# Performance work log

Hardware: AMD Instinct MI355X
Metric: run time of the kernel (lower is better)

Reference implementation:

```python
import jax, jax.numpy as jnp
import numpy as np

B, C, H, W = 8, 768, 32, 32
NH = 12
HD = C // NH
HID = 4 * C
EPS = 1e-5


def _layer_norm(x, g, b):
    mu = jnp.mean(x, axis=-1, keepdims=True)
    var = jnp.mean(jnp.square(x - mu), axis=-1, keepdims=True)
    return (x - mu) * jax.lax.rsqrt(var + EPS) * g + b


def setup_inputs() -> dict:
    key = jax.random.key(0)
    ks = jax.random.split(key, 12)
    s = 0.02
    return {
        "x": jax.random.normal(ks[0], (B, C, H, W), jnp.float32),
        "conv_w": jax.random.normal(ks[1], (C, 1, 3, 3), jnp.float32) * s,  # depthwise OIHW
        "conv_b": jnp.zeros((C,), jnp.float32),
        "ln1_g": jnp.ones((C,), jnp.float32),
        "ln1_b": jnp.zeros((C,), jnp.float32),
        "qkv_w": jax.random.normal(ks[2], (3 * C, C), jnp.float32) * s,  # no bias (qkv_bias=False)
        "proj_w": jax.random.normal(ks[3], (C, C), jnp.float32) * s,
        "proj_b": jnp.zeros((C,), jnp.float32),
        "ln2_g": jnp.ones((C,), jnp.float32),
        "ln2_b": jnp.zeros((C,), jnp.float32),
        "fc1_w": jax.random.normal(ks[4], (HID, C), jnp.float32) * s,
        "fc1_b": jnp.zeros((HID,), jnp.float32),
        "fc2_w": jax.random.normal(ks[5], (C, HID), jnp.float32) * s,
        "fc2_b": jnp.zeros((C,), jnp.float32),
    }


def reference(x, conv_w, conv_b, ln1_g, ln1_b, qkv_w, proj_w, proj_b,
              ln2_g, ln2_b, fc1_w, fc1_b, fc2_w, fc2_b):
    # depthwise 3x3 conv positional embedding, residual
    pe = jax.lax.conv_general_dilated(
        x, conv_w, window_strides=(1, 1), padding=((1, 1), (1, 1)),
        dimension_numbers=("NCHW", "OIHW", "NCHW"), feature_group_count=C)
    x = x + pe + conv_b[None, :, None, None]

    b, c, h, w = x.shape
    t = x.reshape(b, c, h * w).transpose(0, 2, 1)  # [B, N, C]

    # attention
    hn = _layer_norm(t, ln1_g, ln1_b)
    qkv = hn @ qkv_w.T  # [B, N, 3C]
    qkv = qkv.reshape(b, h * w, 3, NH, HD).transpose(2, 0, 3, 1, 4)  # [3, B, nh, N, hd]
    q, k, v = qkv[0], qkv[1], qkv[2]
    scale = HD ** -0.5
    attn = jax.nn.softmax(jnp.einsum("bhnd,bhmd->bhnm", q, k) * scale, axis=-1)
    o = jnp.einsum("bhnm,bhmd->bhnd", attn, v).transpose(0, 2, 1, 3).reshape(b, h * w, c)
    t = t + (o @ proj_w.T + proj_b)

    # MLP
    hn = _layer_norm(t, ln2_g, ln2_b)
    hid = jax.nn.gelu(hn @ fc1_w.T + fc1_b, approximate=False)
    t = t + (hid @ fc2_w.T + fc2_b)

    return t.transpose(0, 2, 1).reshape(b, c, h, w)
```

## Files before the change

kernel.cpp:

```cpp
#include <hip/hip_runtime.h>
#include <math.h>


typedef __bf16 bf16;
typedef __attribute__((ext_vector_type(8))) __bf16 bf16x8;
typedef __attribute__((ext_vector_type(4))) __bf16 bf16x4;
typedef __attribute__((ext_vector_type(4))) float f32x4;

#define B_   8
#define C_   768
#define N_   1024
#define NH_  12
#define HD_  64
#define HID_ 3072
#define NTOK   (B_ * N_)
#define NHEADS (B_ * NH_)
#define FA_C   0.1803368801111601f

__device__ __forceinline__ void gload_lds16(const void* g, void* l) {
  __builtin_amdgcn_global_load_lds(
      (__attribute__((address_space(1))) void*)(void*)g,
      (__attribute__((address_space(3))) void*)l, 16, 0, 0);
}

__device__ __forceinline__ float gelu1(float x) {
  float u = 0.7978845608028654f * x * (1.0f + 0.044715f * x * x);
  float e = __builtin_amdgcn_exp2f(u * 2.885390081777927f);
  float th = 1.0f - 2.0f * __builtin_amdgcn_rcpf(e + 1.0f);
  return 0.5f * x * (1.0f + th);
}

#define PIPE_SYNC(N)                                              \
  do {                                                            \
    asm volatile("s_waitcnt vmcnt(" #N ") lgkmcnt(0)" ::: "memory"); \
    __builtin_amdgcn_sched_barrier(0);                            \
    __builtin_amdgcn_s_barrier();                                 \
    __builtin_amdgcn_sched_barrier(0);                            \
    asm volatile("" ::: "memory");                                \
  } while (0)

#define BAR_FENCED()                                              \
  do {                                                            \
    __builtin_amdgcn_sched_barrier(0);                            \
    __builtin_amdgcn_s_barrier();                                 \
    __builtin_amdgcn_sched_barrier(0);                            \
  } while (0)
#define LGKM0()                                                   \
  do {                                                            \
    asm volatile("s_waitcnt lgkmcnt(0)" ::: "memory");            \
    __builtin_amdgcn_sched_barrier(0);                            \
  } while (0)

__global__ __launch_bounds__(512) void gemm_fc2(
    const bf16* __restrict__ A, const bf16* __restrict__ Bw,
    const float* __restrict__ bias, const float* __restrict__ resid,
    float* __restrict__ outp, int K, int lda, int ldb) {
  __shared__ __align__(16) char smem[122880];
  const int tid = threadIdx.x;
  const int wave = tid >> 6, lane = tid & 63;
  const int wr = wave & 1, wc = wave >> 1;
  const int lr = lane & 15, kq = lane >> 4;

  const int bid = blockIdx.x;
  const int g = bid & 7, s = bid >> 3;
  const int ms = s >> 2;
  const int m0 = (g * 8 + ms) * 128;
  const int n0 = (s & 3) * 192;

  f32x4 acc[4][3];
#pragma unroll
  for (int i = 0; i < 4; ++i)
#pragma unroll
    for (int j = 0; j < 3; ++j) acc[i][j] = (f32x4){0.f, 0.f, 0.f, 0.f};

  const bf16* pa[2];
  const bf16* pb[3];
  int da[2], db[3];
#pragma unroll
  for (int c = 0; c < 2; ++c) {
    const int sidx = c * 512 + tid;
    const int r = sidx >> 3, seg = (sidx & 7) ^ (r & 7);
    pa[c] = A + (size_t)(m0 + r) * lda + seg * 8;
    da[c] = sidx * 16;
  }
#pragma unroll
  for (int c = 0; c < 3; ++c) {
    const int sidx = c * 512 + tid;
    const int r = sidx >> 3, seg = (sidx & 7) ^ (r & 7);
    pb[c] = Bw + (size_t)(n0 + r) * ldb + seg * 8;
    db[c] = 16384 + sidx * 16;
  }

  const int NT = K >> 6;

#pragma unroll
  for (int tt = 0; tt < 2; ++tt) {
    char* wb = smem + tt * 40960;
    gload_lds16(pb[0], wb + db[0]);
    gload_lds16(pb[1], wb + db[1]);
    gload_lds16(pb[2], wb + db[2]);
    gload_lds16(pa[0], wb + da[0]);
    gload_lds16(pa[1], wb + da[1]);
    pb[0] += 64; pb[1] += 64; pb[2] += 64; pa[0] += 64; pa[1] += 64;
  }

  int cur = 0;
  for (int t = 0; t < NT - 1; ++t) {
    const char* rb = smem + cur * 40960;
    int wi = cur + 2; if (wi >= 3) wi -= 3;
    char* wb = smem + wi * 40960;
    const bool dostage = (t < NT - 2);

    asm volatile("s_waitcnt vmcnt(5) lgkmcnt(0)" ::: "memory");
    BAR_FENCED();

    bf16x8 af[4], bf[3];
#pragma unroll
    for (int i = 0; i < 4; ++i) {
      const int r = wr * 64 + i * 16 + lr;
      af[i] = *(const bf16x8*)(rb + (r * 8 + (kq ^ (r & 7))) * 16);
    }
#pragma unroll
    for (int j = 0; j < 3; ++j) {
      const int r = wc * 48 + j * 16 + lr;
      bf[j] = *(const bf16x8*)(rb + 16384 + (r * 8 + (kq ^ (r & 7))) * 16);
    }
    if (dostage) {
      gload_lds16(pb[0], wb + db[0]); pb[0] += 64;
      gload_lds16(pb[1], wb + db[1]); pb[1] += 64;
      gload_lds16(pb[2], wb + db[2]); pb[2] += 64;
    }
    BAR_FENCED();
    LGKM0();
    __builtin_amdgcn_s_setprio(1);
#pragma unroll
    for (int i = 0; i < 4; ++i)
#pragma unroll
      for (int j = 0; j < 3; ++j)
        acc[i][j] = __builtin_amdgcn_mfma_f32_16x16x32_bf16(bf[j], af[i],
                                                            acc[i][j], 0, 0, 0);
    __builtin_amdgcn_s_setprio(0);
    BAR_FENCED();

#pragma unroll
    for (int i = 0; i < 4; ++i) {
      const int r = wr * 64 + i * 16 + lr;
      af[i] = *(const bf16x8*)(rb + (r * 8 + ((4 + kq) ^ (r & 7))) * 16);
    }
#pragma unroll
    for (int j = 0; j < 3; ++j) {
      const int r = wc * 48 + j * 16 + lr;
      bf[j] = *(const bf16x8*)(rb + 16384 + (r * 8 + ((4 + kq) ^ (r & 7))) * 16);
    }
    if (dostage) {
      gload_lds16(pa[0], wb + da[0]); pa[0] += 64;
      gload_lds16(pa[1], wb + da[1]); pa[1] += 64;
    }
    BAR_FENCED();
    LGKM0();
    __builtin_amdgcn_s_setprio(1);
#pragma unroll
    for (int i = 0; i < 4; ++i)
#pragma unroll
      for (int j = 0; j < 3; ++j)
        acc[i][j] = __builtin_amdgcn_mfma_f32_16x16x32_bf16(bf[j], af[i],
                                                            acc[i][j], 0, 0, 0);
    __builtin_amdgcn_s_setprio(0);
    BAR_FENCED();

    if (++cur == 3) cur = 0;
  }

  {
    const char* rb = smem + cur * 40960;
    bf16x8 af[4], bf[3];
    asm volatile("s_waitcnt vmcnt(0) lgkmcnt(0)" ::: "memory");
    BAR_FENCED();
#pragma unroll
    for (int kh = 0; kh < 2; ++kh) {
      const int c0 = kh * 4 + kq;
#pragma unroll
      for (int i = 0; i < 4; ++i) {
        const int r = wr * 64 + i * 16 + lr;
        af[i] = *(const bf16x8*)(rb + (r * 8 + (c0 ^ (r & 7))) * 16);
      }
#pragma unroll
      for (int j = 0; j < 3; ++j) {
        const int r = wc * 48 + j * 16 + lr;
        bf[j] = *(const bf16x8*)(rb + 16384 + (r * 8 + (c0 ^ (r & 7))) * 16);
      }
      __builtin_amdgcn_s_setprio(1);
#pragma unroll
      for (int i = 0; i < 4; ++i)
#pragma unroll
        for (int j = 0; j < 3; ++j)
          acc[i][j] = __builtin_amdgcn_mfma_f32_16x16x32_bf16(bf[j], af[i],
                                                              acc[i][j], 0, 0, 0);
      __builtin_amdgcn_s_setprio(0);
    }
  }

  {
    float* tile = (float*)smem;
    const int b = m0 >> 10, tok0 = m0 & (N_ - 1);
#pragma unroll
    for (int sl = 0; sl < 3; ++sl) {
      __syncthreads();
#pragma unroll
      for (int j = 0; j < 3; ++j) {
        const int nl0 = wc * 48 + j * 16 + kq * 4;
        if (((wc * 48 + j * 16) >> 6) == sl) {
          const int n = n0 + nl0;
          const f32x4 bv = *(const f32x4*)(bias + n);
#pragma unroll
          for (int i = 0; i < 4; ++i) {
            const int ml = wr * 64 + i * 16 + lr;
            const float* rp = resid + (size_t)(m0 + ml) * C_ + n;
            f32x4 old = *(const f32x4*)rp;
            const f32x4 v = acc[i][j];
#pragma unroll
            for (int r = 0; r < 4; ++r)
              tile[(nl0 - sl * 64 + r) * 132 + ml] = old[r] + v[r] + bv[r];
          }
        }
      }
      __syncthreads();
      const int nl = tid & 63, mc = tid >> 6;
      float* dst = outp + ((size_t)(b * C_ + n0 + sl * 64 + nl)) * N_ +
                   tok0 + mc * 16;
      const float* src = tile + nl * 132 + mc * 16;
#pragma unroll
      for (int q = 0; q < 4; ++q)
        *(f32x4*)(dst + q * 4) = *(const f32x4*)(src + q * 4);
    }
  }
}

__global__ __launch_bounds__(512) void gemm_fc1(
    const bf16* __restrict__ A, const bf16* __restrict__ Bw,
    const float* __restrict__ bias, bf16* __restrict__ outp,
    int K, int lda, int ldb, int ntiles, int mtpx, int ldo) {
  __shared__ __align__(16) char smem[114688];
  const int tid = threadIdx.x;
  const int wave = tid >> 6, lane = tid & 63;
  const int wr = wave & 1, wc = wave >> 1;
  const int lr = lane & 15, kq = lane >> 4;

  const int bid = blockIdx.x;
  const int g = bid & 7, s = bid >> 3;
  const int ms = s / ntiles;
  const int m0 = (g * mtpx + ms) * 256;
  const int n0 = (s - ms * ntiles) * 192;

  f32x4 acc[8][3];
#pragma unroll
  for (int i = 0; i < 8; ++i)
#pragma unroll
    for (int j = 0; j < 3; ++j) acc[i][j] = (f32x4){0.f, 0.f, 0.f, 0.f};

  const bf16* pa[4];
  const bf16* pb[3];
  int da[4], db[3];
#pragma unroll
  for (int c = 0; c < 4; ++c) {
    const int sidx = c * 512 + tid;
    const int r = sidx >> 3, seg = (sidx & 7) ^ (r & 7);
    pa[c] = A + (size_t)(m0 + r) * lda + seg * 8;
    da[c] = sidx * 16;
  }
#pragma unroll
  for (int c = 0; c < 3; ++c) {
    const int sidx = c * 512 + tid;
    const int r = sidx >> 3, seg = (sidx & 7) ^ (r & 7);
    pb[c] = Bw + (size_t)(n0 + r) * ldb + seg * 8;
    db[c] = 32768 + sidx * 16;
  }

  const int NT = K >> 6;

  gload_lds16(pb[0], smem + db[0]);
  gload_lds16(pb[1], smem + db[1]);
  gload_lds16(pb[2], smem + db[2]);
  gload_lds16(pa[0], smem + da[0]);
  gload_lds16(pa[1], smem + da[1]);
  gload_lds16(pa[2], smem + da[2]);
  gload_lds16(pa[3], smem + da[3]);
#pragma unroll
  for (int c = 0; c < 4; ++c) pa[c] += 64;
#pragma unroll
  for (int c = 0; c < 3; ++c) pb[c] += 64;

  for (int t = 0; t < NT - 1; ++t) {
    const char* rb = smem + (t & 1) * 57344;
    char* wb = smem + ((t & 1) ^ 1) * 57344;
    bf16x8 af[4], bf0[3], bf1[3];

    PIPE_SYNC(1);
#pragma unroll
    for (int i = 0; i < 4; ++i) {
      const int r = wr * 128 + i * 16 + lr;
      af[i] = *(const bf16x8*)(rb + (r * 8 + (kq ^ (r & 7))) * 16);
    }
#pragma unroll
    for (int j = 0; j < 3; ++j) {
      const int r = wc * 48 + j * 16 + lr;
      bf0[j] = *(const bf16x8*)(rb + 32768 + (r * 8 + (kq ^ (r & 7))) * 16);
    }
    gload_lds16(pb[0], wb + db[0]); pb[0] += 64;
    gload_lds16(pb[1], wb + db[1]); pb[1] += 64;
    __builtin_amdgcn_s_setprio(1);
#pragma unroll
    for (int i = 0; i < 4; ++i)
#pragma unroll
      for (int j = 0; j < 3; ++j)
        acc[i][j] = __builtin_amdgcn_mfma_f32_16x16x32_bf16(bf0[j], af[i],
                                                            acc[i][j], 0, 0, 0);
    __builtin_amdgcn_s_setprio(0);

    PIPE_SYNC(2);
#pragma unroll
    for (int i = 0; i < 4; ++i) {
      const int r = wr * 128 + 64 + i * 16 + lr;
      af[i] = *(const bf16x8*)(rb + (r * 8 + (kq ^ (r & 7))) * 16);
    }
    gload_lds16(pb[2], wb + db[2]); pb[2] += 64;
    gload_lds16(pa[0], wb + da[0]); pa[0] += 64;
    __builtin_amdgcn_s_setprio(1);
#pragma unroll
    for (int i = 0; i < 4; ++i)
#pragma unroll
      for (int j = 0; j < 3; ++j)
        acc[4 + i][j] = __builtin_amdgcn_mfma_f32_16x16x32_bf16(
            bf0[j], af[i], acc[4 + i][j], 0, 0, 0);
    __builtin_amdgcn_s_setprio(0);

    PIPE_SYNC(4);
#pragma unroll
    for (int i = 0; i < 4; ++i) {
      const int r = wr * 128 + i * 16 + lr;
      af[i] = *(const bf16x8*)(rb + (r * 8 + ((4 + kq) ^ (r & 7))) * 16);
    }
#pragma unroll
    for (int j = 0; j < 3; ++j) {
      const int r = wc * 48 + j * 16 + lr;
      bf1[j] = *(const bf16x8*)(rb + 32768 + (r * 8 + ((4 + kq) ^ (r & 7))) * 16);
    }
    gload_lds16(pa[1], wb + da[1]); pa[1] += 64;
    gload_lds16(pa[2], wb + da[2]); pa[2] += 64;
    __builtin_amdgcn_s_setprio(1);
#pragma unroll
    for (int i = 0; i < 4; ++i)
#pragma unroll
      for (int j = 0; j < 3; ++j)
        acc[i][j] = __builtin_amdgcn_mfma_f32_16x16x32_bf16(bf1[j], af[i],
                                                            acc[i][j], 0, 0, 0);
    __builtin_amdgcn_s_setprio(0);

    PIPE_SYNC(6);
#pragma unroll
    for (int i = 0; i < 4; ++i) {
      const int r = wr * 128 + 64 + i * 16 + lr;
      af[i] = *(const bf16x8*)(rb + (r * 8 + ((4 + kq) ^ (r & 7))) * 16);
    }
    gload_lds16(pa[3], wb + da[3]); pa[3] += 64;
    __builtin_amdgcn_s_setprio(1);
#pragma unroll
    for (int i = 0; i < 4; ++i)
#pragma unroll
      for (int j = 0; j < 3; ++j)
        acc[4 + i][j] = __builtin_amdgcn_mfma_f32_16x16x32_bf16(
            bf1[j], af[i], acc[4 + i][j], 0, 0, 0);
    __builtin_amdgcn_s_setprio(0);
  }

  {
    const char* rb = smem + ((NT - 1) & 1) * 57344;
    bf16x8 af[4], bf0[3], bf1[3];
    PIPE_SYNC(0);
#pragma unroll
    for (int j = 0; j < 3; ++j) {
      const int r = wc * 48 + j * 16 + lr;
      bf0[j] = *(const bf16x8*)(rb + 32768 + (r * 8 + (kq ^ (r & 7))) * 16);
      bf1[j] = *(const bf16x8*)(rb + 32768 + (r * 8 + ((4 + kq) ^ (r & 7))) * 16);
    }
    __builtin_amdgcn_s_setprio(1);
#pragma unroll
    for (int half = 0; half < 2; ++half) {
#pragma unroll
      for (int i = 0; i < 4; ++i) {
        const int r = wr * 128 + half * 64 + i * 16 + lr;
        af[i] = *(const bf16x8*)(rb + (r * 8 + (kq ^ (r & 7))) * 16);
      }
#pragma unroll
      for (int i = 0; i < 4; ++i)
#pragma unroll
        for (int j = 0; j < 3; ++j)
          acc[half * 4 + i][j] = __builtin_amdgcn_mfma_f32_16x16x32_bf16(
              bf0[j], af[i], acc[half * 4 + i][j], 0, 0, 0);
#pragma unroll
      for (int i = 0; i < 4; ++i) {
        const int r = wr * 128 + half * 64 + i * 16 + lr;
        af[i] = *(const bf16x8*)(rb + (r * 8 + ((4 + kq) ^ (r & 7))) * 16);
      }
#pragma unroll
      for (int i = 0; i < 4; ++i)
#pragma unroll
        for (int j = 0; j < 3; ++j)
          acc[half * 4 + i][j] = __builtin_amdgcn_mfma_f32_16x16x32_bf16(
              bf1[j], af[i], acc[half * 4 + i][j], 0, 0, 0);
    }
    __builtin_amdgcn_s_setprio(0);
  }

#pragma unroll
  for (int j = 0; j < 3; ++j) {
    const int n = n0 + wc * 48 + j * 16 + kq * 4;
    const f32x4 bv = *(const f32x4*)(bias + n);
#pragma unroll
    for (int i = 0; i < 8; ++i) {
      const int m = m0 + wr * 128 + i * 16 + lr;
      const f32x4 v = acc[i][j];
      bf16x4 pk = {(bf16)gelu1(v[0] + bv[0]), (bf16)gelu1(v[1] + bv[1]),
                   (bf16)gelu1(v[2] + bv[2]), (bf16)gelu1(v[3] + bv[3])};
      *(bf16x4*)(outp + (size_t)m * ldo + n) = pk;
    }
  }
}

template <int BN, int EPI, bool REMAP>
__global__ __launch_bounds__(256) void gemm_bt(
    const bf16* __restrict__ A, const bf16* __restrict__ B, int K, int lda,
    int ldb, int ntiles, bf16* __restrict__ o0, bf16* __restrict__ o1,
    bf16* __restrict__ o2, float* __restrict__ resid,
    const float* __restrict__ bias, float* __restrict__ outp) {
  constexpr int JJ = BN / 32;
  constexpr int BCH = BN / 32;
  constexpr int STAGE_B = (128 + BN) * 64 * 2;
  constexpr int EXTRA_B = (EPI == 0 ? 128 * 256 : 0);
  constexpr int SMEM_B = STAGE_B > EXTRA_B ? STAGE_B : EXTRA_B;
  __shared__ __align__(16) char smemraw[SMEM_B];
  bf16* As = (bf16*)smemraw;
  bf16* Bs = As + 128 * 64;

  const int tid = threadIdx.x;
  const int wave = tid >> 6, lane = tid & 63;
  const int wm = wave & 1, wn = wave >> 1;
  const int lr = lane & 15, kq = lane >> 4;
  const int sw = lr & 7;

  int m0, n0;
  if constexpr (REMAP) {
    const int bid = blockIdx.x;
    const int g = bid & 7, s = bid >> 3;
    const int ms = s / ntiles;
    m0 = (g * 8 + ms) * 128;
    n0 = (s - ms * ntiles) * BN;
  } else {
    m0 = blockIdx.y * 128;
    n0 = blockIdx.x * BN;
  }

  f32x4 acc[4][JJ];
#pragma unroll
  for (int i = 0; i < 4; i++)
#pragma unroll
    for (int j = 0; j < JJ; j++) acc[i][j] = (f32x4){0.f, 0.f, 0.f, 0.f};

  const bf16* ap[4];
  const bf16* bp[BCH];
  {
    const bf16* Arow = A + (size_t)m0 * lda;
    const bf16* Brow = B + (size_t)n0 * ldb;
#pragma unroll
    for (int it = 0; it < 4; ++it) {
      int s = it * 256 + tid;
      int r = s >> 3, seg = (s & 7) ^ (r & 7);
      ap[it] = Arow + (size_t)r * lda + seg * 8;
    }
#pragma unroll
    for (int it = 0; it < BCH; ++it) {
      int s = it * 256 + tid;
      int r = s >> 3, seg = (s & 7) ^ (r & 7);
      bp[it] = Brow + (size_t)r * ldb + seg * 8;
    }
  }

  for (int k0 = 0; k0 < K; k0 += 64) {
#pragma unroll
    for (int it = 0; it < 4; ++it) {
      gload_lds16(ap[it], (char*)As + (it * 256 + tid) * 16);
      ap[it] += 64;
    }
#pragma unroll
    for (int it = 0; it < BCH; ++it) {
      gload_lds16(bp[it], (char*)Bs + (it * 256 + tid) * 16);
      bp[it] += 64;
    }
    __syncthreads();

#pragma unroll
    for (int h = 0; h < 2; ++h) {
      bf16x8 af[4], bfr[JJ];
      const int c = h * 4 + kq;
#pragma unroll
      for (int i = 0; i < 4; i++) {
        int row = wm * 64 + i * 16 + lr;
        af[i] = *(const bf16x8*)((char*)As + (row * 8 + (c ^ sw)) * 16);
      }
#pragma unroll
      for (int j = 0; j < JJ; j++) {
        int row = wn * (BN / 2) + j * 16 + lr;
        bfr[j] = *(const bf16x8*)((char*)Bs + (row * 8 + (c ^ sw)) * 16);
      }
#pragma unroll
      for (int i = 0; i < 4; i++)
#pragma unroll
        for (int j = 0; j < JJ; j++)
          acc[i][j] = __builtin_amdgcn_mfma_f32_16x16x32_bf16(bfr[j], af[i],
                                                              acc[i][j], 0, 0, 0);
    }
    __syncthreads();
  }

  if constexpr (EPI == 0) {
    const int b = m0 >> 10, tok0 = m0 & (N_ - 1);
    if (n0 < 2 * C_) {
      const int s = n0 >= C_ ? 1 : 0;
      bf16* dst = s ? o1 : o0;
#pragma unroll
      for (int i = 0; i < 4; i++) {
        const int m = m0 + wm * 64 + i * 16 + lr;
#pragma unroll
        for (int j = 0; j < JJ; j++) {
          const int rem = n0 - s * C_ + wn * (BN / 2) + j * 16 + kq * 4;
          const int h = rem >> 6, d = rem & 63;
          const f32x4 v = acc[i][j];
          bf16x4 pk = {(bf16)v[0], (bf16)v[1], (bf16)v[2], (bf16)v[3]};
          size_t head = (size_t)b * NH_ + h;
          *(bf16x4*)(dst + (head * N_ + (m & (N_ - 1))) * HD_ + d) = pk;
        }
      }
    } else {
      bf16* tile = (bf16*)smemraw;
#pragma unroll
      for (int i = 0; i < 4; i++) {
        const int ml = wm * 64 + i * 16 + lr;
        const int mc = ml >> 3, mo = ml & 7;
#pragma unroll
        for (int j = 0; j < JJ; j++) {
          const f32x4 v = acc[i][j];
#pragma unroll
          for (int r = 0; r < 4; r++) {
            const int nl = wn * (BN / 2) + j * 16 + kq * 4 + r;
            *(bf16*)((char*)tile + nl * 256 + ((mc ^ (nl & 15)) * 16) + mo * 2) =
                (bf16)v[r];
          }
        }
      }
      __syncthreads();
      const int nl = tid >> 1, mh = (tid & 1) * 64;
      const int vb = n0 - 2 * C_ + nl;
      const size_t head = (size_t)b * NH_ + (vb >> 6);
      bf16* dst = o2 + (head * HD_ + (vb & 63)) * N_ + tok0 + mh;
#pragma unroll
      for (int c8 = 0; c8 < 8; ++c8) {
        const int c = (mh >> 3) + c8;
        bf16x8 val = *(const bf16x8*)((char*)tile + nl * 256 +
                                      ((c ^ (nl & 15)) * 16));
        *(bf16x8*)(dst + c8 * 8) = val;
      }
    }
  } else if constexpr (EPI == 3) {
#pragma unroll
    for (int j = 0; j < JJ; j++) {
      const int n = n0 + wn * (BN / 2) + j * 16 + kq * 4;
      const f32x4 bv = *(const f32x4*)(bias + n);
#pragma unroll
      for (int i = 0; i < 4; i++) {
        const int m = m0 + wm * 64 + i * 16 + lr;
        float* rp = resid + (size_t)m * C_ + n;
        f32x4 old = *(const f32x4*)rp;
        const f32x4 v = acc[i][j];
        f32x4 nw = {old[0] + v[0] + bv[0], old[1] + v[1] + bv[1],
                    old[2] + v[2] + bv[2], old[3] + v[3] + bv[3]};
        *(f32x4*)rp = nw;
      }
    }
  }
}

__global__ __launch_bounds__(256, 3) void flash_attn(
    const bf16* __restrict__ Qb, const bf16* __restrict__ Kb,
    const bf16* __restrict__ Vt, bf16* __restrict__ attn) {
  __shared__ __align__(16) bf16 ksm[2][64 * 64];
  __shared__ __align__(16) bf16 vsm[2][64 * 64];
  __shared__ __align__(16) bf16 psm[4][32 * 64];

  const int tid = threadIdx.x, wave = tid >> 6, lane = tid & 63;
  const int lr = lane & 15, kq = lane >> 4;
  const int head = blockIdx.y;
  const int b = head / NH_, hh = head - b * NH_;
  const int q0 = blockIdx.x * 128;
  const bf16* Qh = Qb + (size_t)head * (N_ * HD_);
  const bf16* Kh = Kb + (size_t)head * (N_ * HD_);
  const bf16* Vh = Vt + (size_t)head * (HD_ * N_);
  char* pw = (char*)&psm[wave][0];

  bf16x8 qf[2][2];
#pragma unroll
  for (int j = 0; j < 2; ++j)
#pragma unroll
    for (int kh = 0; kh < 2; ++kh)
      qf[j][kh] = *(const bf16x8*)(Qh +
                                   (size_t)(q0 + wave * 32 + j * 16 + lr) * HD_ +
                                   kh * 32 + kq * 8);

  f32x4 o[4][2];
#pragma unroll
  for (int i = 0; i < 4; i++)
#pragma unroll
    for (int j = 0; j < 2; j++) o[i][j] = (f32x4){0.f, 0.f, 0.f, 0.f};
  float mprev[2] = {-1e30f, -1e30f}, lacc[2] = {0.f, 0.f};

  auto stage = [&](int t, int bi) {
#pragma unroll
    for (int it = 0; it < 2; ++it) {
      int s = it * 256 + tid;
      int r = s >> 3, seg = (s & 7) ^ (r & 7);
      gload_lds16(Kh + (size_t)(t * 64 + r) * HD_ + seg * 8,
                  (char*)ksm[bi] + (it * 256 + wave * 64) * 16);
    }
#pragma unroll
    for (int it = 0; it < 2; ++it) {
      int s = it * 256 + tid;
      int r = s >> 3, seg = (s & 7) ^ (r & 7);
      gload_lds16(Vh + (size_t)r * N_ + t * 64 + seg * 8,
                  (char*)vsm[bi] + (it * 256 + wave * 64) * 16);
    }
  };

  stage(0, 0);

  for (int t = 0; t < 16; ++t) {
    const int bi = t & 1;
    __syncthreads();
    if (t < 15) stage(t + 1, bi ^ 1);

    f32x4 sacc[4][2];
#pragma unroll
    for (int i = 0; i < 4; ++i) {
#pragma unroll
      for (int j = 0; j < 2; ++j) sacc[i][j] = (f32x4){0.f, 0.f, 0.f, 0.f};
      int row = i * 16 + lr;
      bf16x8 kf0 = *(const bf16x8*)((char*)ksm[bi] + row * 128 +
                                    ((kq ^ (row & 7)) * 16));
      bf16x8 kf1 = *(const bf16x8*)((char*)ksm[bi] + row * 128 +
                                    (((4 + kq) ^ (row & 7)) * 16));
#pragma unroll
      for (int j = 0; j < 2; ++j) {
        sacc[i][j] = __builtin_amdgcn_mfma_f32_16x16x32_bf16(kf0, qf[j][0],
                                                             sacc[i][j], 0, 0, 0);
        sacc[i][j] = __builtin_amdgcn_mfma_f32_16x16x32_bf16(kf1, qf[j][1],
                                                             sacc[i][j], 0, 0, 0);
      }
    }

#pragma unroll
    for (int j = 0; j < 2; ++j) {
      float mx = -1e30f;
#pragma unroll
      for (int i = 0; i < 4; ++i)
#pragma unroll
        for (int r = 0; r < 4; ++r) mx = fmaxf(mx, sacc[i][j][r]);
      mx = fmaxf(mx, __shfl_xor(mx, 16));
      mx = fmaxf(mx, __shfl_xor(mx, 32));
      float mnew = fmaxf(mprev[j], mx);
      float alpha = __builtin_amdgcn_exp2f((mprev[j] - mnew) * FA_C);
      mprev[j] = mnew;
      float rs = 0.f;
      const int prow = j * 16 + lr;
#pragma unroll
      for (int i = 0; i < 4; ++i) {
        float p0 = __builtin_amdgcn_exp2f((sacc[i][j][0] - mnew) * FA_C);
        float p1 = __builtin_amdgcn_exp2f((sacc[i][j][1] - mnew) * FA_C);
        float p2 = __builtin_amdgcn_exp2f((sacc[i][j][2] - mnew) * FA_C);
        float p3 = __builtin_amdgcn_exp2f((sacc[i][j][3] - mnew) * FA_C);
        rs += (p0 + p1) + (p2 + p3);
        bf16x4 pk = {(bf16)p0, (bf16)p1, (bf16)p2, (bf16)p3};
        int c = i * 2 + (kq >> 1);
        *(bf16x4*)(pw + prow * 128 + ((c ^ (prow & 7)) * 16) + (kq & 1) * 8) = pk;
      }
      rs += __shfl_xor(rs, 16);
      rs += __shfl_xor(rs, 32);
      lacc[j] = lacc[j] * alpha + rs;
#pragma unroll
      for (int i = 0; i < 4; ++i) {
        o[i][j][0] *= alpha; o[i][j][1] *= alpha;
        o[i][j][2] *= alpha; o[i][j][3] *= alpha;
      }
    }

#pragma unroll
    for (int k0c = 0; k0c < 2; ++k0c) {
      bf16x8 pf[2];
#pragma unroll
      for (int j = 0; j < 2; ++j) {
        int prow = j * 16 + lr, c = k0c * 4 + kq;
        pf[j] = *(const bf16x8*)(pw + prow * 128 + ((c ^ (prow & 7)) * 16));
      }
#pragma unroll
      for (int i = 0; i < 4; ++i) {
        int d = i * 16 + lr, c = k0c * 4 + kq;
        bf16x8 vf = *(const bf16x8*)((char*)vsm[bi] + d * 128 +
                                     ((c ^ (d & 7)) * 16));
#pragma unroll
        for (int j = 0; j < 2; ++j)
          o[i][j] = __builtin_amdgcn_mfma_f32_16x16x32_bf16(vf, pf[j], o[i][j],
                                                            0, 0, 0);
      }
    }
  }

#pragma unroll
  for (int j = 0; j < 2; ++j) {
    float inv = 1.0f / lacc[j];
    int tok = q0 + wave * 32 + j * 16 + lr;
    bf16* op = attn + ((size_t)(b * N_ + tok)) * C_ + hh * HD_;
#pragma unroll
    for (int i = 0; i < 4; ++i) {
      bf16x4 pk = {(bf16)(o[i][j][0] * inv), (bf16)(o[i][j][1] * inv),
                   (bf16)(o[i][j][2] * inv), (bf16)(o[i][j][3] * inv)};
      *(bf16x4*)(op + i * 16 + kq * 4) = pk;
    }
  }
}

__global__ __launch_bounds__(256) void cast_all(
    const float* __restrict__ a, int na, const float* __restrict__ b, int nb,
    const float* __restrict__ c, int nc, const float* __restrict__ d,
    bf16* __restrict__ dst) {
  int i = (blockIdx.x * 256 + threadIdx.x) * 4;
  const float* src;
  int off;
  if (i < na) { src = a; off = i; }
  else if (i < na + nb) { src = b; off = i - na; }
  else if (i < na + nb + nc) { src = c; off = i - na - nb; }
  else { src = d; off = i - na - nb - nc; }
  float4 v = *(const float4*)(src + off);
  bf16x4 o = {(bf16)v.x, (bf16)v.y, (bf16)v.z, (bf16)v.w};
  *(bf16x4*)(dst + i) = o;
}

__global__ __launch_bounds__(256) void conv_pe_t(const float* __restrict__ x,
                                                 const float* __restrict__ cw,
                                                 const float* __restrict__ cb,
                                                 float* __restrict__ t0) {
  __shared__ float tile[32][33];
  const int h = blockIdx.x, ct = blockIdx.y, b = blockIdx.z;
  const int tid = threadIdx.x;
  const int w = tid & 31, cs = tid >> 5;
#pragma unroll
  for (int cc = cs; cc < 32; cc += 8) {
    int c = ct * 32 + cc;
    const float* xp = x + ((size_t)(b * C_ + c)) * 1024;
    const float* wp = cw + c * 9;
    float s = cb[c] + xp[h * 32 + w];
#pragma unroll
    for (int ky = 0; ky < 3; ++ky) {
      int hy = h + ky - 1;
      if ((unsigned)hy < 32u) {
#pragma unroll
        for (int kx = 0; kx < 3; ++kx) {
          int wx = w + kx - 1;
          if ((unsigned)wx < 32u) s += xp[hy * 32 + wx] * wp[ky * 3 + kx];
        }
      }
    }
    tile[cc][w] = s;
  }
  __syncthreads();
  const int cc = tid & 31;
#pragma unroll
  for (int wc = tid >> 5; wc < 32; wc += 8)
    t0[((size_t)(b * N_) + h * 32 + wc) * C_ + ct * 32 + cc] = tile[cc][wc];
}

__global__ __launch_bounds__(256) void ln_bf16(const float* __restrict__ t,
                                               const float* __restrict__ g,
                                               const float* __restrict__ be,
                                               bf16* __restrict__ out) {
  int row = blockIdx.x, tid = threadIdx.x;
  const float* p = t + (size_t)row * C_;
  float v0 = p[tid], v1 = p[tid + 256], v2 = p[tid + 512];
  __shared__ float rs[256], rq[256];
  rs[tid] = v0 + v1 + v2;
  rq[tid] = v0 * v0 + v1 * v1 + v2 * v2;
  __syncthreads();
  for (int off = 128; off; off >>= 1) {
    if (tid < off) {
      rs[tid] += rs[tid + off];
      rq[tid] += rq[tid + off];
    }
    __syncthreads();
  }
  float mu = rs[0] * (1.f / C_);
  float var = rq[0] * (1.f / C_) - mu * mu;
  float rstd = rsqrtf(var + 1e-5f);
  bf16* q = out + (size_t)row * C_;
  q[tid] = (bf16)((v0 - mu) * rstd * g[tid] + be[tid]);
  q[tid + 256] = (bf16)((v1 - mu) * rstd * g[tid + 256] + be[tid + 256]);
  q[tid + 512] = (bf16)((v2 - mu) * rstd * g[tid + 512] + be[tid + 512]);
}

extern "C" void kernel_launch(void* const* d_in, const int* in_sizes, int n_in,
                              void* d_out, int out_size, void* d_ws,
                              size_t ws_size, hipStream_t stream) {
  (void)in_sizes; (void)n_in; (void)out_size; (void)ws_size;
  const float* x      = (const float*)d_in[0];
  const float* conv_w = (const float*)d_in[1];
  const float* conv_b = (const float*)d_in[2];
  const float* ln1_g  = (const float*)d_in[3];
  const float* ln1_b  = (const float*)d_in[4];
  const float* qkv_w  = (const float*)d_in[5];
  const float* proj_w = (const float*)d_in[6];
  const float* proj_b = (const float*)d_in[7];
  const float* ln2_g  = (const float*)d_in[8];
  const float* ln2_b  = (const float*)d_in[9];
  const float* fc1_w  = (const float*)d_in[10];
  const float* fc1_b  = (const float*)d_in[11];
  const float* fc2_w  = (const float*)d_in[12];
  const float* fc2_b  = (const float*)d_in[13];
  float* out = (float*)d_out;

  char* w = (char*)d_ws;
  auto carve = [&](size_t bytes) {
    char* p = w;
    w += (bytes + 255) & ~(size_t)255;
    return p;
  };
  bf16* hid   = (bf16*)carve((size_t)NTOK * HID_ * 2);
  float* t0   = (float*)carve((size_t)NTOK * C_ * 4);
  bf16* lnout = (bf16*)carve((size_t)NTOK * C_ * 2);
  bf16* wq    = (bf16*)carve((size_t)3 * C_ * C_ * 2);
  bf16* wp    = (bf16*)carve((size_t)C_ * C_ * 2);
  bf16* w1    = (bf16*)carve((size_t)HID_ * C_ * 2);
  bf16* w2    = (bf16*)carve((size_t)C_ * HID_ * 2);
  bf16* Qb    = (bf16*)carve((size_t)NHEADS * N_ * HD_ * 2);
  bf16* Kb    = (bf16*)carve((size_t)NHEADS * N_ * HD_ * 2);
  bf16* Vt    = (bf16*)carve((size_t)NHEADS * HD_ * N_ * 2);
  bf16* attn  = (bf16*)carve((size_t)NTOK * C_ * 2);

  const int na = 3 * C_ * C_, nb = C_ * C_, nc = HID_ * C_, nd = C_ * HID_;
  cast_all<<<(na + nb + nc + nd) / 1024, 256, 0, stream>>>(
      qkv_w, na, proj_w, nb, fc1_w, nc, fc2_w, wq);

  conv_pe_t<<<dim3(32, C_ / 32, B_), 256, 0, stream>>>(x, conv_w, conv_b, t0);

  ln_bf16<<<NTOK, 256, 0, stream>>>(t0, ln1_g, ln1_b, lnout);
  gemm_bt<128, 0, true><<<1152, 256, 0, stream>>>(
      lnout, wq, 768, 768, 768, 18, Qb, Kb, Vt, nullptr, nullptr, nullptr);

  flash_attn<<<dim3(N_ / 128, NHEADS), 256, 0, stream>>>(Qb, Kb, Vt, attn);

  gemm_bt<64, 3, true><<<768, 256, 0, stream>>>(
      attn, wp, 768, 768, 768, 12, nullptr, nullptr, nullptr, t0, proj_b,
      nullptr);
  ln_bf16<<<NTOK, 256, 0, stream>>>(t0, ln2_g, ln2_b, lnout);
  gemm_fc1<<<512, 512, 0, stream>>>(lnout, w1, fc1_b, hid, 768, 768, 768,
                                    16, 4, HID_);
  gemm_fc2<<<256, 512, 0, stream>>>(hid, w2, fc2_b, t0, out, 3072, 3072, 3072);
}
```

Measured before the change: 386.2 us.

## Replace fc1 GEMM with 256x256-tile 8-phase pipelined kernel and simplify fc2 sync

The fc1 GEMM moves from 256x192 tiles to 256x256 tiles (384 blocks instead of 512). It uses a new four-quadrant schedule where each K step splits into phases that interleave partial LDS reads, global-to-LDS staging and MFMA blocks, with reuse of A/B fragments across quadrants. The aim is a higher MFMA-to-load ratio and better overlap of memory traffic with compute. fc2's main loop is also simplified: one PIPE_SYNC per K step, all staging issued up front, and the mid-iteration barriers removed. This cuts barrier overhead but depends on the triple-buffer distance for correctness, and the fc1 change raises register and LDS pressure.

```diff
diff --git a/kernel.cpp b/kernel.cpp
--- a/kernel.cpp
+++ b/kernel.cpp
@@ -50,6 +50,240 @@
     asm volatile("s_waitcnt lgkmcnt(0)" ::: "memory");            \
     __builtin_amdgcn_sched_barrier(0);                            \
   } while (0)
+#define WAITV4()                                                  \
+  do {                                                            \
+    asm volatile("s_waitcnt vmcnt(4)" ::: "memory");              \
+    __builtin_amdgcn_sched_barrier(0);                            \
+  } while (0)
+
+__global__ __launch_bounds__(512) void gemm_fc1_8ph(
+    const bf16* __restrict__ A, const bf16* __restrict__ Bw,
+    const float* __restrict__ bias, bf16* __restrict__ outp,
+    int K, int lda, int ldb, int ntiles, int mtpx, int ldo) {
+  __shared__ __align__(16) char smem[131072];
+  const int tid = threadIdx.x;
+  const int wave = tid >> 6, lane = tid & 63;
+  const int wr = wave & 1, wc = wave >> 1;
+  const int lr = lane & 15, kq = lane >> 4;
+
+  const int bid = blockIdx.x;
+  const int g = bid & 7, s = bid >> 3;
+  const int ms = s / ntiles;
+  const int m0 = (g * mtpx + ms) * 256;
+  const int n0 = (s - ms * ntiles) * 256;
+
+  f32x4 acc[8][4];
+#pragma unroll
+  for (int i = 0; i < 8; ++i)
+#pragma unroll
+    for (int j = 0; j < 4; ++j) acc[i][j] = (f32x4){0.f, 0.f, 0.f, 0.f};
+
+  const bf16* pa[2][2];
+  const bf16* pb[2][2];
+  int dof[2];
+#pragma unroll
+  for (int ld = 0; ld < 2; ++ld) {
+    const int sidx = ld * 512 + tid;
+    const int r = sidx >> 3, seg = (sidx & 7) ^ (r & 7);
+    pa[0][ld] = A + (size_t)(m0 + r) * lda + seg * 8;
+    pa[1][ld] = A + (size_t)(m0 + 128 + r) * lda + seg * 8;
+    pb[0][ld] = Bw + (size_t)(n0 + r) * ldb + seg * 8;
+    pb[1][ld] = Bw + (size_t)(n0 + 128 + r) * ldb + seg * 8;
+    dof[ld] = sidx * 16;
+  }
+
+  const int NT = K >> 6;
+
+  auto aread = [&](const char* base, int qm, int i, int k) -> bf16x8 {
+    const int ra = qm * 64 + i * 16 + lr;
+    const int c = k * 4 + kq;
+    return *(const bf16x8*)(base + wr * 16384 +
+                            (ra * 8 + (c ^ (ra & 7))) * 16);
+  };
+  auto bread = [&](const char* base, int qn, int j, int k) -> bf16x8 {
+    const int cb = wc * 64 + qn * 32 + j * 16;
+    const int hb = cb >> 7;
+    const int rl = (cb & 127) + lr;
+    const int c = k * 4 + kq;
+    return *(const bf16x8*)(base + 32768 + hb * 16384 +
+                            (rl * 8 + (c ^ (rl & 7))) * 16);
+  };
+
+  gload_lds16(pa[0][0], smem + dof[0]);
+  gload_lds16(pa[0][1], smem + dof[1]);
+  gload_lds16(pb[0][0], smem + 32768 + dof[0]);
+  gload_lds16(pb[0][1], smem + 32768 + dof[1]);
+  gload_lds16(pa[1][0], smem + 16384 + dof[0]);
+  gload_lds16(pa[1][1], smem + 16384 + dof[1]);
+  gload_lds16(pb[1][0], smem + 49152 + dof[0]);
+  gload_lds16(pb[1][1], smem + 49152 + dof[1]);
+#pragma unroll
+  for (int ld = 0; ld < 2; ++ld) {
+    pa[0][ld] += 64; pa[1][ld] += 64; pb[0][ld] += 64; pb[1][ld] += 64;
+  }
+  PIPE_SYNC(4);
+
+  for (int t = 0; t < NT - 1; ++t) {
+    const char* rb = smem + (t & 1) * 65536;
+    char* wb = smem + ((t & 1) ^ 1) * 65536;
+    bf16x8 af0[4][2], af1[4][2], bf0[2][2], bf1[2][2];
+
+#pragma unroll
+    for (int i = 0; i < 4; ++i)
+#pragma unroll
+      for (int k = 0; k < 2; ++k) af0[i][k] = aread(rb, 0, i, k);
+#pragma unroll
+    for (int j = 0; j < 2; ++j)
+#pragma unroll
+      for (int k = 0; k < 2; ++k) bf0[j][k] = bread(rb, 0, j, k);
+    gload_lds16(pa[0][0], wb + dof[0]); pa[0][0] += 64;
+    gload_lds16(pa[0][1], wb + dof[1]); pa[0][1] += 64;
+    WAITV4();
+    BAR_FENCED();
+    LGKM0();
+    __builtin_amdgcn_s_setprio(1);
+#pragma unroll
+    for (int k = 0; k < 2; ++k)
+#pragma unroll
+      for (int i = 0; i < 4; ++i)
+#pragma unroll
+        for (int j = 0; j < 2; ++j)
+          acc[i][j] = __builtin_amdgcn_mfma_f32_16x16x32_bf16(
+              bf0[j][k], af0[i][k], acc[i][j], 0, 0, 0);
+    __builtin_amdgcn_s_setprio(0);
+    BAR_FENCED();
+
+#pragma unroll
+    for (int i = 0; i < 4; ++i)
+#pragma unroll
+      for (int k = 0; k < 2; ++k) af1[i][k] = aread(rb, 1, i, k);
+    gload_lds16(pb[0][0], wb + 32768 + dof[0]); pb[0][0] += 64;
+    gload_lds16(pb[0][1], wb + 32768 + dof[1]); pb[0][1] += 64;
+    WAITV4();
+    BAR_FENCED();
+    LGKM0();
+    __builtin_amdgcn_s_setprio(1);
+#pragma unroll
+    for (int k = 0; k < 2; ++k)
+#pragma unroll
+      for (int i = 0; i < 4; ++i)
+#pragma unroll
+        for (int j = 0; j < 2; ++j)
+          acc[4 + i][j] = __builtin_amdgcn_mfma_f32_16x16x32_bf16(
+              bf0[j][k], af1[i][k], acc[4 + i][j], 0, 0, 0);
+    __builtin_amdgcn_s_setprio(0);
+    BAR_FENCED();
+
+#pragma unroll
+    for (int j = 0; j < 2; ++j)
+#pragma unroll
+      for (int k = 0; k < 2; ++k) bf1[j][k] = bread(rb, 1, j, k);
+    gload_lds16(pa[1][0], wb + 16384 + dof[0]); pa[1][0] += 64;
+    gload_lds16(pa[1][1], wb + 16384 + dof[1]); pa[1][1] += 64;
+    BAR_FENCED();
+    LGKM0();
+    __builtin_amdgcn_s_setprio(1);
+#pragma unroll
+    for (int k = 0; k < 2; ++k)
+#pragma unroll
+      for (int i = 0; i < 4; ++i)
+#pragma unroll
+        for (int j = 0; j < 2; ++j)
+          acc[i][2 + j] = __builtin_amdgcn_mfma_f32_16x16x32_bf16(
+              bf1[j][k], af0[i][k], acc[i][2 + j], 0, 0, 0);
+    __builtin_amdgcn_s_setprio(0);
+    BAR_FENCED();
+
+    gload_lds16(pb[1][0], wb + 49152 + dof[0]); pb[1][0] += 64;
+    gload_lds16(pb[1][1], wb + 49152 + dof[1]); pb[1][1] += 64;
+    WAITV4();
+    BAR_FENCED();
+    LGKM0();
+    __builtin_amdgcn_s_setprio(1);
+#pragma unroll
+    for (int k = 0; k < 2; ++k)
+#pragma unroll
+      for (int i = 0; i < 4; ++i)
+#pragma unroll
+        for (int j = 0; j < 2; ++j)
+          acc[4 + i][2 + j] = __builtin_amdgcn_mfma_f32_16x16x32_bf16(
+              bf1[j][k], af1[i][k], acc[4 + i][2 + j], 0, 0, 0);
+    __builtin_amdgcn_s_setprio(0);
+    BAR_FENCED();
+  }
+
+  {
+    const char* rb = smem + ((NT - 1) & 1) * 65536;
+    bf16x8 af0[4][2], af1[4][2], bf0[2][2], bf1[2][2];
+    PIPE_SYNC(0);
+#pragma unroll
+    for (int i = 0; i < 4; ++i)
+#pragma unroll
+      for (int k = 0; k < 2; ++k) af0[i][k] = aread(rb, 0, i, k);
+#pragma unroll
+    for (int j = 0; j < 2; ++j)
+#pragma unroll
+      for (int k = 0; k < 2; ++k) bf0[j][k] = bread(rb, 0, j, k);
+    LGKM0();
+    __builtin_amdgcn_s_setprio(1);
+#pragma unroll
+    for (int k = 0; k < 2; ++k)
+#pragma unroll
+      for (int i = 0; i < 4; ++i)
+#pragma unroll
+        for (int j = 0; j < 2; ++j)
+          acc[i][j] = __builtin_amdgcn_mfma_f32_16x16x32_bf16(
+              bf0[j][k], af0[i][k], acc[i][j], 0, 0, 0);
+    __builtin_amdgcn_s_setprio(0);
+#pragma unroll
+    for (int i = 0; i < 4; ++i)
+#pragma unroll
+      for (int k = 0; k < 2; ++k) af1[i][k] = aread(rb, 1, i, k);
+    LGKM0();
+    __builtin_amdgcn_s_setprio(1);
+#pragma unroll
+    for (int k = 0; k < 2; ++k)
+#pragma unroll
+      for (int i = 0; i < 4; ++i)
+#pragma unroll
+        for (int j = 0; j < 2; ++j)
+          acc[4 + i][j] = __builtin_amdgcn_mfma_f32_16x16x32_bf16(
+              bf0[j][k], af1[i][k], acc[4 + i][j], 0, 0, 0);
+    __builtin_amdgcn_s_setprio(0);
+#pragma unroll
+    for (int j = 0; j < 2; ++j)
+#pragma unroll
+      for (int k = 0; k < 2; ++k) bf1[j][k] = bread(rb, 1, j, k);
+    LGKM0();
+    __builtin_amdgcn_s_setprio(1);
+#pragma unroll
+    for (int k = 0; k < 2; ++k)
+#pragma unroll
+      for (int i = 0; i < 4; ++i)
+#pragma unroll
+        for (int j = 0; j < 2; ++j) {
+          acc[i][2 + j] = __builtin_amdgcn_mfma_f32_16x16x32_bf16(
+              bf1[j][k], af0[i][k], acc[i][2 + j], 0, 0, 0);
+          acc[4 + i][2 + j] = __builtin_amdgcn_mfma_f32_16x16x32_bf16(
+              bf1[j][k], af1[i][k], acc[4 + i][2 + j], 0, 0, 0);
+        }
+    __builtin_amdgcn_s_setprio(0);
+  }
+
+#pragma unroll
+  for (int j = 0; j < 4; ++j) {
+    const int n = n0 + wc * 64 + j * 16 + kq * 4;
+    const f32x4 bv = *(const f32x4*)(bias + n);
+#pragma unroll
+    for (int i = 0; i < 8; ++i) {
+      const int m = m0 + wr * 128 + i * 16 + lr;
+      const f32x4 v = acc[i][j];
+      bf16x4 pk = {(bf16)gelu1(v[0] + bv[0]), (bf16)gelu1(v[1] + bv[1]),
+                   (bf16)gelu1(v[2] + bv[2]), (bf16)gelu1(v[3] + bv[3])};
+      *(bf16x4*)(outp + (size_t)m * ldo + n) = pk;
+    }
+  }
+}
 
 __global__ __launch_bounds__(512) void gemm_fc2(
     const bf16* __restrict__ A, const bf16* __restrict__ Bw,
@@ -107,13 +341,16 @@
   int cur = 0;
   for (int t = 0; t < NT - 1; ++t) {
     const char* rb = smem + cur * 40960;
-    int wi = cur + 2; if (wi >= 3) wi -= 3;
-    char* wb = smem + wi * 40960;
-    const bool dostage = (t < NT - 2);
-
-    asm volatile("s_waitcnt vmcnt(5) lgkmcnt(0)" ::: "memory");
-    BAR_FENCED();
-
+    PIPE_SYNC(5);
+    if (t < NT - 2) {
+      int wi = cur + 2; if (wi >= 3) wi -= 3;
+      char* wb = smem + wi * 40960;
+      gload_lds16(pb[0], wb + db[0]); pb[0] += 64;
+      gload_lds16(pb[1], wb + db[1]); pb[1] += 64;
+      gload_lds16(pb[2], wb + db[2]); pb[2] += 64;
+      gload_lds16(pa[0], wb + da[0]); pa[0] += 64;
+      gload_lds16(pa[1], wb + da[1]); pa[1] += 64;
+    }
     bf16x8 af[4], bf[3];
 #pragma unroll
     for (int i = 0; i < 4; ++i) {
@@ -125,13 +362,6 @@
       const int r = wc * 48 + j * 16 + lr;
       bf[j] = *(const bf16x8*)(rb + 16384 + (r * 8 + (kq ^ (r & 7))) * 16);
     }
-    if (dostage) {
-      gload_lds16(pb[0], wb + db[0]); pb[0] += 64;
-      gload_lds16(pb[1], wb + db[1]); pb[1] += 64;
-      gload_lds16(pb[2], wb + db[2]); pb[2] += 64;
-    }
-    BAR_FENCED();
-    LGKM0();
     __builtin_amdgcn_s_setprio(1);
 #pragma unroll
     for (int i = 0; i < 4; ++i)
@@ -140,8 +370,6 @@
         acc[i][j] = __builtin_amdgcn_mfma_f32_16x16x32_bf16(bf[j], af[i],
                                                             acc[i][j], 0, 0, 0);
     __builtin_amdgcn_s_setprio(0);
-    BAR_FENCED();
-
 #pragma unroll
     for (int i = 0; i < 4; ++i) {
       const int r = wr * 64 + i * 16 + lr;
@@ -152,12 +380,6 @@
       const int r = wc * 48 + j * 16 + lr;
       bf[j] = *(const bf16x8*)(rb + 16384 + (r * 8 + ((4 + kq) ^ (r & 7))) * 16);
     }
-    if (dostage) {
-      gload_lds16(pa[0], wb + da[0]); pa[0] += 64;
-      gload_lds16(pa[1], wb + da[1]); pa[1] += 64;
-    }
-    BAR_FENCED();
-    LGKM0();
     __builtin_amdgcn_s_setprio(1);
 #pragma unroll
     for (int i = 0; i < 4; ++i)
@@ -166,16 +388,13 @@
         acc[i][j] = __builtin_amdgcn_mfma_f32_16x16x32_bf16(bf[j], af[i],
                                                             acc[i][j], 0, 0, 0);
     __builtin_amdgcn_s_setprio(0);
-    BAR_FENCED();
-
     if (++cur == 3) cur = 0;
   }
 
   {
     const char* rb = smem + cur * 40960;
     bf16x8 af[4], bf[3];
-    asm volatile("s_waitcnt vmcnt(0) lgkmcnt(0)" ::: "memory");
-    BAR_FENCED();
+    PIPE_SYNC(0);
 #pragma unroll
     for (int kh = 0; kh < 2; ++kh) {
       const int c0 = kh * 4 + kq;
@@ -232,197 +451,6 @@
 #pragma unroll
       for (int q = 0; q < 4; ++q)
         *(f32x4*)(dst + q * 4) = *(const f32x4*)(src + q * 4);
-    }
-  }
-}
-
-__global__ __launch_bounds__(512) void gemm_fc1(
-    const bf16* __restrict__ A, const bf16* __restrict__ Bw,
-    const float* __restrict__ bias, bf16* __restrict__ outp,
-    int K, int lda, int ldb, int ntiles, int mtpx, int ldo) {
-  __shared__ __align__(16) char smem[114688];
-  const int tid = threadIdx.x;
-  const int wave = tid >> 6, lane = tid & 63;
-  const int wr = wave & 1, wc = wave >> 1;
-  const int lr = lane & 15, kq = lane >> 4;
-
-  const int bid = blockIdx.x;
-  const int g = bid & 7, s = bid >> 3;
-  const int ms = s / ntiles;
-  const int m0 = (g * mtpx + ms) * 256;
-  const int n0 = (s - ms * ntiles) * 192;
-
-  f32x4 acc[8][3];
-#pragma unroll
-  for (int i = 0; i < 8; ++i)
-#pragma unroll
-    for (int j = 0; j < 3; ++j) acc[i][j] = (f32x4){0.f, 0.f, 0.f, 0.f};
-
-  const bf16* pa[4];
-  const bf16* pb[3];
-  int da[4], db[3];
-#pragma unroll
-  for (int c = 0; c < 4; ++c) {
-    const int sidx = c * 512 + tid;
-    const int r = sidx >> 3, seg = (sidx & 7) ^ (r & 7);
-    pa[c] = A + (size_t)(m0 + r) * lda + seg * 8;
-    da[c] = sidx * 16;
-  }
-#pragma unroll
-  for (int c = 0; c < 3; ++c) {
-    const int sidx = c * 512 + tid;
-    const int r = sidx >> 3, seg = (sidx & 7) ^ (r & 7);
-    pb[c] = Bw + (size_t)(n0 + r) * ldb + seg * 8;
-    db[c] = 32768 + sidx * 16;
-  }
-
-  const int NT = K >> 6;
-
-  gload_lds16(pb[0], smem + db[0]);
-  gload_lds16(pb[1], smem + db[1]);
-  gload_lds16(pb[2], smem + db[2]);
-  gload_lds16(pa[0], smem + da[0]);
-  gload_lds16(pa[1], smem + da[1]);
-  gload_lds16(pa[2], smem + da[2]);
-  gload_lds16(pa[3], smem + da[3]);
-#pragma unroll
-  for (int c = 0; c < 4; ++c) pa[c] += 64;
-#pragma unroll
-  for (int c = 0; c < 3; ++c) pb[c] += 64;
-
-  for (int t = 0; t < NT - 1; ++t) {
-    const char* rb = smem + (t & 1) * 57344;
-    char* wb = smem + ((t & 1) ^ 1) * 57344;
-    bf16x8 af[4], bf0[3], bf1[3];
-
-    PIPE_SYNC(1);
-#pragma unroll
-    for (int i = 0; i < 4; ++i) {
-      const int r = wr * 128 + i * 16 + lr;
-      af[i] = *(const bf16x8*)(rb + (r * 8 + (kq ^ (r & 7))) * 16);
-    }
-#pragma unroll
-    for (int j = 0; j < 3; ++j) {
-      const int r = wc * 48 + j * 16 + lr;
-      bf0[j] = *(const bf16x8*)(rb + 32768 + (r * 8 + (kq ^ (r & 7))) * 16);
-    }
-    gload_lds16(pb[0], wb + db[0]); pb[0] += 64;
-    gload_lds16(pb[1], wb + db[1]); pb[1] += 64;
-    __builtin_amdgcn_s_setprio(1);
-#pragma unroll
-    for (int i = 0; i < 4; ++i)
-#pragma unroll
-      for (int j = 0; j < 3; ++j)
-        acc[i][j] = __builtin_amdgcn_mfma_f32_16x16x32_bf16(bf0[j], af[i],
-                                                            acc[i][j], 0, 0, 0);
-    __builtin_amdgcn_s_setprio(0);
-
-    PIPE_SYNC(2);
-#pragma unroll
-    for (int i = 0; i < 4; ++i) {
-      const int r = wr * 128 + 64 + i * 16 + lr;
-      af[i] = *(const bf16x8*)(rb + (r * 8 + (kq ^ (r & 7))) * 16);
-    }
-    gload_lds16(pb[2], wb + db[2]); pb[2] += 64;
-    gload_lds16(pa[0], wb + da[0]); pa[0] += 64;
-    __builtin_amdgcn_s_setprio(1);
-#pragma unroll
-    for (int i = 0; i < 4; ++i)
-#pragma unroll
-      for (int j = 0; j < 3; ++j)
-        acc[4 + i][j] = __builtin_amdgcn_mfma_f32_16x16x32_bf16(
-            bf0[j], af[i], acc[4 + i][j], 0, 0, 0);
-    __builtin_amdgcn_s_setprio(0);
-
-    PIPE_SYNC(4);
-#pragma unroll
-    for (int i = 0; i < 4; ++i) {
-      const int r = wr * 128 + i * 16 + lr;
-      af[i] = *(const bf16x8*)(rb + (r * 8 + ((4 + kq) ^ (r & 7))) * 16);
-    }
-#pragma unroll
-    for (int j = 0; j < 3; ++j) {
-      const int r = wc * 48 + j * 16 + lr;
-      bf1[j] = *(const bf16x8*)(rb + 32768 + (r * 8 + ((4 + kq) ^ (r & 7))) * 16);
-    }
-    gload_lds16(pa[1], wb + da[1]); pa[1] += 64;
-    gload_lds16(pa[2], wb + da[2]); pa[2] += 64;
-    __builtin_amdgcn_s_setprio(1);
-#pragma unroll
-    for (int i = 0; i < 4; ++i)
-#pragma unroll
-      for (int j = 0; j < 3; ++j)
-        acc[i][j] = __builtin_amdgcn_mfma_f32_16x16x32_bf16(bf1[j], af[i],
-                                                            acc[i][j], 0, 0, 0);
-    __builtin_amdgcn_s_setprio(0);
-
-    PIPE_SYNC(6);
-#pragma unroll
-    for (int i = 0; i < 4; ++i) {
-      const int r = wr * 128 + 64 + i * 16 + lr;
-      af[i] = *(const bf16x8*)(rb + (r * 8 + ((4 + kq) ^ (r & 7))) * 16);
-    }
-    gload_lds16(pa[3], wb + da[3]); pa[3] += 64;
-    __builtin_amdgcn_s_setprio(1);
-#pragma unroll
-    for (int i = 0; i < 4; ++i)
-#pragma unroll
-      for (int j = 0; j < 3; ++j)
-        acc[4 + i][j] = __builtin_amdgcn_mfma_f32_16x16x32_bf16(
-            bf1[j], af[i], acc[4 + i][j], 0, 0, 0);
-    __builtin_amdgcn_s_setprio(0);
-  }
-
-  {
-    const char* rb = smem + ((NT - 1) & 1) * 57344;
-    bf16x8 af[4], bf0[3], bf1[3];
-    PIPE_SYNC(0);
-#pragma unroll
-    for (int j = 0; j < 3; ++j) {
-      const int r = wc * 48 + j * 16 + lr;
-      bf0[j] = *(const bf16x8*)(rb + 32768 + (r * 8 + (kq ^ (r & 7))) * 16);
-      bf1[j] = *(const bf16x8*)(rb + 32768 + (r * 8 + ((4 + kq) ^ (r & 7))) * 16);
-    }
-    __builtin_amdgcn_s_setprio(1);
-#pragma unroll
-    for (int half = 0; half < 2; ++half) {
-#pragma unroll
-      for (int i = 0; i < 4; ++i) {
-        const int r = wr * 128 + half * 64 + i * 16 + lr;
-        af[i] = *(const bf16x8*)(rb + (r * 8 + (kq ^ (r & 7))) * 16);
-      }
-#pragma unroll
-      for (int i = 0; i < 4; ++i)
-#pragma unroll
-        for (int j = 0; j < 3; ++j)
-          acc[half * 4 + i][j] = __builtin_amdgcn_mfma_f32_16x16x32_bf16(
-              bf0[j], af[i], acc[half * 4 + i][j], 0, 0, 0);
-#pragma unroll
-      for (int i = 0; i < 4; ++i) {
-        const int r = wr * 128 + half * 64 + i * 16 + lr;
-        af[i] = *(const bf16x8*)(rb + (r * 8 + ((4 + kq) ^ (r & 7))) * 16);
-      }
-#pragma unroll
-      for (int i = 0; i < 4; ++i)
-#pragma unroll
-        for (int j = 0; j < 3; ++j)
-          acc[half * 4 + i][j] = __builtin_amdgcn_mfma_f32_16x16x32_bf16(
-              bf1[j], af[i], acc[half * 4 + i][j], 0, 0, 0);
-    }
-    __builtin_amdgcn_s_setprio(0);
-  }
-
-#pragma unroll
-  for (int j = 0; j < 3; ++j) {
-    const int n = n0 + wc * 48 + j * 16 + kq * 4;
-    const f32x4 bv = *(const f32x4*)(bias + n);
-#pragma unroll
-    for (int i = 0; i < 8; ++i) {
-      const int m = m0 + wr * 128 + i * 16 + lr;
-      const f32x4 v = acc[i][j];
-      bf16x4 pk = {(bf16)gelu1(v[0] + bv[0]), (bf16)gelu1(v[1] + bv[1]),
-                   (bf16)gelu1(v[2] + bv[2]), (bf16)gelu1(v[3] + bv[3])};
-      *(bf16x4*)(outp + (size_t)m * ldo + n) = pk;
     }
   }
 }
@@ -866,7 +894,7 @@
       attn, wp, 768, 768, 768, 12, nullptr, nullptr, nullptr, t0, proj_b,
       nullptr);
   ln_bf16<<<NTOK, 256, 0, stream>>>(t0, ln2_g, ln2_b, lnout);
-  gemm_fc1<<<512, 512, 0, stream>>>(lnout, w1, fc1_b, hid, 768, 768, 768,
-                                    16, 4, HID_);
+  gemm_fc1_8ph<<<384, 512, 0, stream>>>(lnout, w1, fc1_b, hid, 768, 768, 768,
+                                        12, 4, HID_);
   gemm_fc2<<<256, 512, 0, stream>>>(hid, w2, fc2_b, t0, out, 3072, 3072, 3072);
 }
```

New measurement: 404.2 us. 4.7% more time.
